# Optimization experiments

Measured on AMD Instinct MI355X. Metric: run time of the kernel, lower is better.

The kernel has to match this reference:

```python
import jax, jax.numpy as jnp
import numpy as np

HIDDEN = 1024
HEADS = 16
HEAD_DIM = HIDDEN // HEADS
ROPE_THETA = 10000.0
WINDOW = 128
NEG_INF = -1e9


def _rope_cos_sin(seq_len, head_dim, theta, dtype):
    # inv_freq: [dh/2]; emb = concat([freqs, freqs]) to match rotate-half convention
    inv_freq = 1.0 / (theta ** (jnp.arange(0, head_dim, 2, dtype=jnp.float32) / head_dim))
    pos = jnp.arange(seq_len, dtype=jnp.float32)
    freqs = jnp.einsum('s,d->sd', pos, inv_freq)          # [S, dh/2]
    emb = jnp.concatenate([freqs, freqs], axis=-1)        # [S, dh]
    return jnp.cos(emb).astype(dtype), jnp.sin(emb).astype(dtype)


def _apply_rope(x, cos, sin):
    # x: [B, S, H, dh]; cos/sin: [S, dh] broadcast over batch and heads
    x1, x2 = jnp.split(x, 2, axis=-1)
    half_rot = jnp.concatenate([-x2, x1], axis=-1)
    c = cos[None, :, None, :]
    s = sin[None, :, None, :]
    return x * c + half_rot * s


def setup_inputs() -> dict:
    key = jax.random.key(0)
    k1, k2, k3, k4, k5 = jax.random.split(key, 5)
    std = 0.02
    return {
        'hidden_states': jax.random.normal(k1, (2, 2048, HIDDEN), dtype=jnp.float32),
        'Wq': jax.random.normal(k2, (HIDDEN, HEADS, HEAD_DIM), dtype=jnp.float32) * std,
        'Wk': jax.random.normal(k3, (HIDDEN, HEADS, HEAD_DIM), dtype=jnp.float32) * std,
        'Wv': jax.random.normal(k4, (HIDDEN, HEADS, HEAD_DIM), dtype=jnp.float32) * std,
        'Wo': jax.random.normal(k5, (HEADS, HEAD_DIM, HIDDEN), dtype=jnp.float32) * std,
    }


def reference(hidden_states, Wq, Wk, Wv, Wo):
    B, S, D = hidden_states.shape
    x4 = hidden_states.reshape(B, S, HEADS, HEAD_DIM)
    cos, sin = _rope_cos_sin(S, HEAD_DIM, ROPE_THETA, hidden_states.dtype)
    # RoPE applied to raw hidden states (pre-projection), per original module
    q_in = _apply_rope(x4, cos, sin).reshape(B, S, D)
    k_in = q_in  # query and key get identical RoPE of the same tensor
    v_in = hidden_states

    q = jnp.einsum('bsd,dhk->bshk', q_in, Wq)  # [B,S,H,dh]
    k = jnp.einsum('bsd,dhk->bshk', k_in, Wk)
    v = jnp.einsum('bsd,dhk->bshk', v_in, Wv)

    scale = 1.0 / jnp.sqrt(jnp.asarray(HEAD_DIM, dtype=q.dtype))
    scores = jnp.einsum('bqhd,bkhd->bhqk', q, k) * scale  # [B,H,S,S]

    # sliding-window mask: |i - j| < WINDOW
    pos = jnp.arange(S)
    win = jnp.abs(pos[:, None] - pos[None, :]) < WINDOW   # [S,S] bool
    scores = jnp.where(win[None, None, :, :], scores, NEG_INF)

    probs = jax.nn.softmax(scores, axis=-1)
    out = jnp.einsum('bhqk,bkhd->bqhd', probs, v)          # [B,S,H,dh]
    return jnp.einsum('bqhd,hdo->bqo', out, Wo)            # [B,S,D]
```

## Files before the change

kernel.cpp:

```cpp
#include <hip/hip_runtime.h>
#include <hip/hip_bf16.h>
#include <cstdint>
#include <cmath>

typedef __bf16 bf16_t;
typedef __bf16 bf16x8 __attribute__((ext_vector_type(8)));
typedef __bf16 bf16x4 __attribute__((ext_vector_type(4)));
typedef float  f32x4  __attribute__((ext_vector_type(4)));

#define MFMA16(a, b, c) __builtin_amdgcn_mfma_f32_16x16x32_bf16(a, b, c, 0, 0, 0)

constexpr int   SS    = 2048;
constexpr int   DD    = 1024;
constexpr int   HH    = 16;
constexpr float SCALE = 0.125f;
constexpr float L2E   = 1.44269504088896f;

__device__ __forceinline__ bool detect_fp32(const uint16_t* w) {
    uint16_t v = w[threadIdx.x & 63];
    int e = (v >> 7) & 0xFF;
    unsigned long long m = __ballot(e >= 0x80);
    return __popcll(m) >= 4;
}

__device__ __forceinline__ float ldin(const void* p, size_t i, bool f32) {
    return f32 ? ((const float*)p)[i] : (float)((const bf16_t*)p)[i];
}

__device__ __forceinline__ void gload_lds16(const bf16_t* g, bf16_t* l) {
    __builtin_amdgcn_global_load_lds(
        (const __attribute__((address_space(1))) void*)(g),
        (__attribute__((address_space(3))) void*)(l), 16, 0, 0);
}

__global__ __launch_bounds__(256) void prep_kernel(
    const void* __restrict__ hidden, const void* __restrict__ Wq,
    const void* __restrict__ Wk, const void* __restrict__ Wv,
    const void* __restrict__ Wo,
    bf16_t* __restrict__ roped, bf16_t* __restrict__ hiddenb,
    bf16_t* __restrict__ WqT, bf16_t* __restrict__ WkT,
    bf16_t* __restrict__ WvT, bf16_t* __restrict__ WoT) {
    const bool f32 = detect_fp32((const uint16_t*)Wq);
    __shared__ bf16_t tile[32][33];
    if (blockIdx.x < 1024) {
        int gid = blockIdx.x * 256 + threadIdx.x;
        int ic = (gid & 3) * 8;
        int h  = (gid >> 2) & 15;
        int s  = (gid >> 6) & 2047;
        int b  = gid >> 17;
        size_t base = ((size_t)(b * SS + s)) * DD + h * 64 + ic;
        float x[8], y[8];
        if (f32) {
            const float* hp = (const float*)hidden;
            f32x4 x0 = *(const f32x4*)(hp + base);
            f32x4 x1 = *(const f32x4*)(hp + base + 4);
            f32x4 y0 = *(const f32x4*)(hp + base + 32);
            f32x4 y1 = *(const f32x4*)(hp + base + 36);
#pragma unroll
            for (int j = 0; j < 4; ++j) {
                x[j] = x0[j]; x[4 + j] = x1[j];
                y[j] = y0[j]; y[4 + j] = y1[j];
            }
        } else {
            const bf16_t* hp = (const bf16_t*)hidden;
            bf16x8 xv = *(const bf16x8*)(hp + base);
            bf16x8 yv = *(const bf16x8*)(hp + base + 32);
#pragma unroll
            for (int j = 0; j < 8; ++j) { x[j] = (float)xv[j]; y[j] = (float)yv[j]; }
        }
        bf16x8 ro, rh;
#pragma unroll
        for (int j = 0; j < 8; ++j) {
            int i = ic + j;
            float invf = exp2f(-(float)i * (13.287712379549449f / 32.0f));
            float sn, cs;
            __sincosf((float)s * invf, &sn, &cs);
            ro[j]  = (bf16_t)(x[j] * cs - y[j] * sn);
            rh[j]  = (bf16_t)(y[j] * cs + x[j] * sn);
        }
        *(bf16x8*)(roped + base)      = ro;
        *(bf16x8*)(roped + base + 32) = rh;
        if (f32) {
            bf16x8 hb0, hb1;
#pragma unroll
            for (int j = 0; j < 8; ++j) { hb0[j] = (bf16_t)x[j]; hb1[j] = (bf16_t)y[j]; }
            *(bf16x8*)(hiddenb + base)      = hb0;
            *(bf16x8*)(hiddenb + base + 32) = hb1;
        }
    } else {
        int w = blockIdx.x - 1024;
        int z = w >> 10;
        int yy = (w >> 5) & 31, xx = w & 31;
        const void* src = (z == 0) ? Wq : (z == 1) ? Wk : (z == 2) ? Wv : Wo;
        bf16_t*     dst = (z == 0) ? WqT : (z == 1) ? WkT : (z == 2) ? WvT : WoT;
        int tx = threadIdx.x & 31, ty = threadIdx.x >> 5;
        int x0 = xx * 32, y0 = yy * 32;
#pragma unroll
        for (int j = 0; j < 4; ++j)
            tile[ty + j * 8][tx] =
                (bf16_t)ldin(src, (size_t)(y0 + ty + j * 8) * DD + x0 + tx, f32);
        __syncthreads();
#pragma unroll
        for (int j = 0; j < 4; ++j)
            dst[(size_t)(x0 + ty + j * 8) * DD + y0 + tx] = tile[tx][ty + j * 8];
    }
}

__device__ __forceinline__ void stage_a128(const bf16_t* A, int m0, int k0,
                                           bf16_t* As, int tid) {
#pragma unroll
    for (int i = 0; i < 4; ++i) {
        int c = tid + i * 256;
        int r = c >> 3, g = (c & 7) ^ (r & 7);
        gload_lds16(A + (size_t)(m0 + r) * DD + k0 + g * 8, As + c * 8);
    }
}
__device__ __forceinline__ void stage_b64(const bf16_t* Bt, int n0, int k0,
                                          bf16_t* Bs, int tid) {
#pragma unroll
    for (int i = 0; i < 2; ++i) {
        int c = tid + i * 256;
        int r = c >> 3, g = (c & 7) ^ (r & 7);
        gload_lds16(Bt + (size_t)(n0 + r) * DD + k0 + g * 8, Bs + c * 8);
    }
}

__global__ __launch_bounds__(256, 4) void gemm_qkv_fused(
    const bf16_t* __restrict__ roped, const void* __restrict__ hidden_raw,
    const bf16_t* __restrict__ hiddenb, const uint16_t* __restrict__ wdet,
    const bf16_t* __restrict__ WqT, const bf16_t* __restrict__ WkT,
    const bf16_t* __restrict__ WvT,
    bf16_t* __restrict__ Qo, bf16_t* __restrict__ Ko, bf16_t* __restrict__ Vt) {
    __shared__ __align__(16) bf16_t As[128 * 64];
    __shared__ __align__(16) bf16_t B1[64 * 64];
    __shared__ __align__(16) bf16_t B2[64 * 64];
    const int tid = threadIdx.x, lane = tid & 63, quad = lane >> 4, l16 = lane & 15;
    const int wave = tid >> 6, wm = (wave >> 1) * 64, wn = (wave & 1) * 32;
    const int sw = l16 & 7;

    const int lin = blockIdx.x;
    const int z   = lin & 1;
    const int p   = lin >> 1;
    const int xcd = p & 7, rem = p >> 3;
    const int mb  = (xcd >> 1) * 8 + (rem >> 3);
    const int nb  = (xcd & 1) * 8 + (rem & 7);
    const int m0  = mb * 128, n0 = nb * 64;

    f32x4 acc1[4][2], acc2[4][2];
#pragma unroll
    for (int i = 0; i < 4; ++i)
#pragma unroll
        for (int j = 0; j < 2; ++j) { acc1[i][j] = (f32x4)0.0f; acc2[i][j] = (f32x4)0.0f; }

    if (z == 0) {
        for (int k0 = 0; k0 < DD; k0 += 64) {
            stage_a128(roped, m0, k0, As, tid);
            stage_b64(WqT, n0, k0, B1, tid);
            stage_b64(WkT, n0, k0, B2, tid);
            __syncthreads();
#pragma unroll
            for (int half = 0; half < 2; ++half) {
                const int h4 = half * 4;
                bf16x8 af[4], b1f[2], b2f[2];
#pragma unroll
                for (int t = 0; t < 4; ++t)
                    af[t] = *(const bf16x8*)(As + (wm + t * 16 + l16) * 64 + ((h4 + quad) ^ sw) * 8);
#pragma unroll
                for (int t = 0; t < 2; ++t) {
                    b1f[t] = *(const bf16x8*)(B1 + (wn + t * 16 + l16) * 64 + ((h4 + quad) ^ sw) * 8);
                    b2f[t] = *(const bf16x8*)(B2 + (wn + t * 16 + l16) * 64 + ((h4 + quad) ^ sw) * 8);
                }
#pragma unroll
                for (int i = 0; i < 4; ++i)
#pragma unroll
                    for (int j = 0; j < 2; ++j) {
                        acc1[i][j] = MFMA16(af[i], b1f[j], acc1[i][j]);
                        acc2[i][j] = MFMA16(af[i], b2f[j], acc2[i][j]);
                    }
            }
            __syncthreads();
        }
#pragma unroll
        for (int i = 0; i < 4; ++i) {
            int mbase = m0 + wm + i * 16 + quad * 4;
            int b = mbase >> 11, sl = mbase & 2047;
#pragma unroll
            for (int j = 0; j < 2; ++j) {
                int d = wn + j * 16 + l16;
                size_t base = (((size_t)b * HH + nb) * SS + sl) * 64 + d;
#pragma unroll
                for (int r = 0; r < 4; ++r) {
                    Qo[base + 64 * r] = (bf16_t)acc1[i][j][r];
                    Ko[base + 64 * r] = (bf16_t)acc2[i][j][r];
                }
            }
        }
    } else {
        const bool f32 = detect_fp32(wdet);
        const bf16_t* A = f32 ? hiddenb : (const bf16_t*)hidden_raw;
        for (int k0 = 0; k0 < DD; k0 += 64) {
            stage_a128(A, m0, k0, As, tid);
            stage_b64(WvT, n0, k0, B1, tid);
            __syncthreads();
#pragma unroll
            for (int half = 0; half < 2; ++half) {
                const int h4 = half * 4;
                bf16x8 af[4], b1f[2];
#pragma unroll
                for (int t = 0; t < 4; ++t)
                    af[t] = *(const bf16x8*)(As + (wm + t * 16 + l16) * 64 + ((h4 + quad) ^ sw) * 8);
#pragma unroll
                for (int t = 0; t < 2; ++t)
                    b1f[t] = *(const bf16x8*)(B1 + (wn + t * 16 + l16) * 64 + ((h4 + quad) ^ sw) * 8);
#pragma unroll
                for (int i = 0; i < 4; ++i)
#pragma unroll
                    for (int j = 0; j < 2; ++j)
                        acc1[i][j] = MFMA16(af[i], b1f[j], acc1[i][j]);
            }
            __syncthreads();
        }
#pragma unroll
        for (int i = 0; i < 4; ++i) {
            int mbase = m0 + wm + i * 16 + quad * 4;
            int b = mbase >> 11, sl = mbase & 2047;
#pragma unroll
            for (int j = 0; j < 2; ++j) {
                int d = wn + j * 16 + l16;
                bf16x4 v;
                v[0] = (bf16_t)acc1[i][j][0]; v[1] = (bf16_t)acc1[i][j][1];
                v[2] = (bf16_t)acc1[i][j][2]; v[3] = (bf16_t)acc1[i][j][3];
                *(bf16x4*)(Vt + (((size_t)b * HH + nb) * 64 + d) * SS + sl) = v;
            }
        }
    }
}

__global__ __launch_bounds__(256) void attn_kernel(
    const bf16_t* __restrict__ Q, const bf16_t* __restrict__ Kk,
    const bf16_t* __restrict__ Vt, bf16_t* __restrict__ attn) {
    __shared__ __align__(16) bf16_t Ks[2][32 * 64];
    __shared__ __align__(16) bf16_t Vs[2][64 * 32];
    __shared__ __align__(16) bf16_t Pl[4][16 * 40];
    const int tid = threadIdx.x, wave = tid >> 6, lane = tid & 63;
    const int quad = lane >> 4, l16 = lane & 15;
    const int sw7 = l16 & 7, sw3 = l16 & 3;

    int lin = (blockIdx.x >> 3) + 128 * (blockIdx.x & 7);
    const int qb0 = (lin & 31) * 64;
    const int h   = (lin >> 5) & 15;
    const int b   = lin >> 9;
    const int qw  = qb0 + wave * 16;

    const size_t bh = (size_t)b * HH + h;
    const bf16_t* Qp = Q  + bh * SS * 64;
    const bf16_t* Kp = Kk + bh * SS * 64;
    const bf16_t* Vp = Vt + bh * 64 * SS;
    bf16_t* P = &Pl[wave][0];

    bf16x8 q0 = *(const bf16x8*)(Qp + (size_t)(qw + l16) * 64 + quad * 8);
    bf16x8 q1 = *(const bf16x8*)(Qp + (size_t)(qw + l16) * 64 + 32 + quad * 8);

    f32x4 Oacc[4];
#pragma unroll
    for (int t = 0; t < 4; ++t) Oacc[t] = (f32x4)0.0f;
    float lsum[4] = {0.f, 0.f, 0.f, 0.f};

    int lo = qb0 - 127; if (lo < 0) lo = 0; lo &= ~31;
    int hi = qb0 + 63 + 127; if (hi > SS - 1) hi = SS - 1;

    const int krow = tid >> 3, kcol = ((tid & 7) ^ (krow & 7)) * 8;
    const int vrow = tid >> 2, vcol = ((tid & 3) ^ (vrow & 3)) * 8;

    int parity = 0;
    for (int kt = lo; kt <= hi; kt += 32, parity ^= 1) {
        gload_lds16(Kp + (size_t)(kt + krow) * 64 + kcol, &Ks[parity][0] + tid * 8);
        gload_lds16(Vp + (size_t)vrow * SS + kt + vcol, &Vs[parity][0] + tid * 8);
        __syncthreads();

        const bf16_t* Kl = &Ks[parity][0];
        const bf16_t* Vl = &Vs[parity][0];
        bf16x8 k00 = *(const bf16x8*)(Kl + l16 * 64 + (quad ^ sw7) * 8);
        bf16x8 k01 = *(const bf16x8*)(Kl + l16 * 64 + ((quad + 4) ^ sw7) * 8);
        bf16x8 k10 = *(const bf16x8*)(Kl + (16 + l16) * 64 + (quad ^ sw7) * 8);
        bf16x8 k11 = *(const bf16x8*)(Kl + (16 + l16) * 64 + ((quad + 4) ^ sw7) * 8);
        bf16x8 vf[4];
#pragma unroll
        for (int t = 0; t < 4; ++t)
            vf[t] = *(const bf16x8*)(Vl + (t * 16 + l16) * 32 + (quad ^ sw3) * 8);

        f32x4 s0 = MFMA16(q0, k00, (f32x4)0.0f);  s0 = MFMA16(q1, k01, s0);
        f32x4 s1 = MFMA16(q0, k10, (f32x4)0.0f);  s1 = MFMA16(q1, k11, s1);

        const int kr0 = kt + l16, kr1 = kt + 16 + l16;
#pragma unroll
        for (int r = 0; r < 4; ++r) {
            int qa = qw + quad * 4 + r;
            int d0 = qa - kr0; if (d0 < 0) d0 = -d0;
            int d1 = qa - kr1; if (d1 < 0) d1 = -d1;
            float p0 = (d0 < 128) ? exp2f(s0[r] * (SCALE * L2E)) : 0.0f;
            float p1 = (d1 < 128) ? exp2f(s1[r] * (SCALE * L2E)) : 0.0f;
            lsum[r] += p0 + p1;
            P[(quad * 4 + r) * 40 + l16]      = (bf16_t)p0;
            P[(quad * 4 + r) * 40 + 16 + l16] = (bf16_t)p1;
        }
        __asm__ volatile("s_waitcnt lgkmcnt(0)" ::: "memory");
        bf16x8 pf = *(const bf16x8*)(P + l16 * 40 + quad * 8);
#pragma unroll
        for (int t = 0; t < 4; ++t)
            Oacc[t] = MFMA16(pf, vf[t], Oacc[t]);
    }

#pragma unroll
    for (int r = 0; r < 4; ++r) {
        float l = lsum[r];
        l += __shfl_xor(l, 1, 64);
        l += __shfl_xor(l, 2, 64);
        l += __shfl_xor(l, 4, 64);
        l += __shfl_xor(l, 8, 64);
        float inv = 1.0f / l;
        int sa = qw + quad * 4 + r;
        size_t base = (((size_t)b * SS + sa) * HH + h) * 64 + l16;
        attn[base]      = (bf16_t)(Oacc[0][r] * inv);
        attn[base + 16] = (bf16_t)(Oacc[1][r] * inv);
        attn[base + 32] = (bf16_t)(Oacc[2][r] * inv);
        attn[base + 48] = (bf16_t)(Oacc[3][r] * inv);
    }
}

__global__ __launch_bounds__(256, 4) void gemm_out_kernel(
    const bf16_t* __restrict__ A, const bf16_t* __restrict__ WoT,
    const uint16_t* __restrict__ wdet, void* __restrict__ out) {
    __shared__ __align__(16) bf16_t As[128 * 64];
    __shared__ __align__(16) bf16_t B1[64 * 64];
    const int tid = threadIdx.x, lane = tid & 63, quad = lane >> 4, l16 = lane & 15;
    const int wave = tid >> 6, wm = (wave >> 1) * 64, wn = (wave & 1) * 32;
    const int sw = l16 & 7;

    const int lin = blockIdx.x;
    const int xcd = lin & 7, s = lin >> 3;
    const int mb = (xcd >> 1) * 8 + (s >> 3);
    const int nb = (xcd & 1) * 8 + (s & 7);
    const int m0 = mb * 128, n0 = nb * 64;

    f32x4 acc[4][2];
#pragma unroll
    for (int i = 0; i < 4; ++i)
#pragma unroll
        for (int j = 0; j < 2; ++j) acc[i][j] = (f32x4)0.0f;

    for (int k0 = 0; k0 < DD; k0 += 64) {
        stage_a128(A, m0, k0, As, tid);
        stage_b64(WoT, n0, k0, B1, tid);
        __syncthreads();
#pragma unroll
        for (int half = 0; half < 2; ++half) {
            const int h4 = half * 4;
            bf16x8 af[4], b1f[2];
#pragma unroll
            for (int t = 0; t < 4; ++t)
                af[t] = *(const bf16x8*)(As + (wm + t * 16 + l16) * 64 + ((h4 + quad) ^ sw) * 8);
#pragma unroll
            for (int t = 0; t < 2; ++t)
                b1f[t] = *(const bf16x8*)(B1 + (wn + t * 16 + l16) * 64 + ((h4 + quad) ^ sw) * 8);
#pragma unroll
            for (int i = 0; i < 4; ++i)
#pragma unroll
                for (int j = 0; j < 2; ++j)
                    acc[i][j] = MFMA16(af[i], b1f[j], acc[i][j]);
        }
        __syncthreads();
    }

    const bool f32 = detect_fp32(wdet);
#pragma unroll
    for (int i = 0; i < 4; ++i) {
        int mbase = m0 + wm + i * 16 + quad * 4;
#pragma unroll
        for (int j = 0; j < 2; ++j) {
            int n = n0 + wn + j * 16 + l16;
#pragma unroll
            for (int r = 0; r < 4; ++r) {
                size_t idx = (size_t)(mbase + r) * DD + n;
                if (f32) ((float*)out)[idx] = acc[i][j][r];
                else     ((bf16_t*)out)[idx] = (bf16_t)acc[i][j][r];
            }
        }
    }
}

extern "C" void kernel_launch(void* const* d_in, const int* in_sizes, int n_in,
                              void* d_out, int out_size, void* d_ws, size_t ws_size,
                              hipStream_t stream) {
    const void* hidden = d_in[0];
    const void* Wq = d_in[1];
    const void* Wk = d_in[2];
    const void* Wv = d_in[3];
    const void* Wo = d_in[4];
    const uint16_t* wdet = (const uint16_t*)d_in[1];
    char* ws = (char*)d_ws;

    bf16_t* roped   = (bf16_t*)(ws);
    bf16_t* hiddenb = (bf16_t*)(ws + ( 8u << 20));
    bf16_t* WqT     = (bf16_t*)(ws + (16u << 20));
    bf16_t* WkT     = (bf16_t*)(ws + (18u << 20));
    bf16_t* WvT     = (bf16_t*)(ws + (20u << 20));
    bf16_t* WoT     = (bf16_t*)(ws + (22u << 20));
    bf16_t* Qb      = (bf16_t*)(ws + (24u << 20));
    bf16_t* Kb      = (bf16_t*)(ws + (32u << 20));
    bf16_t* Vt      = (bf16_t*)(ws + (40u << 20));
    bf16_t* attn    = roped;

    hipLaunchKernelGGL(prep_kernel, dim3(5120), dim3(256), 0, stream,
                       hidden, Wq, Wk, Wv, Wo, roped, hiddenb,
                       WqT, WkT, WvT, WoT);
    hipLaunchKernelGGL(gemm_qkv_fused, dim3(1024), dim3(256), 0, stream,
                       roped, hidden, hiddenb, wdet, WqT, WkT, WvT, Qb, Kb, Vt);
    hipLaunchKernelGGL(attn_kernel, dim3(1024), dim3(256), 0, stream,
                       Qb, Kb, Vt, attn);
    hipLaunchKernelGGL(gemm_out_kernel, dim3(512), dim3(256), 0, stream,
                       attn, WoT, wdet, d_out);
}
```

Before: 153.4 us.

## Retile QKV GEMM to uniform 128x128 tiles and add MFMA priority hints

The QKV projection kernel drops the mixed Q+K-fused and V blocks. Every block now computes a uniform 128x128 output tile for one of Q, K or V, over a 768-block grid, with each wave holding 4x4 accumulators. This balances the work per block and raises arithmetic intensity per LDS load, at the cost of more registers and a lower occupancy bound (3 blocks per CU instead of 4). The attention kernel also wraps its MFMA groups in s_setprio to favour the matrix-issuing waves.

Measured after the change: 157.8 us. 1.03x slower.

```diff
diff --git a/kernel.cpp b/kernel.cpp
--- a/kernel.cpp
+++ b/kernel.cpp
@@ -125,112 +125,92 @@
     }
 }
 
-__global__ __launch_bounds__(256, 4) void gemm_qkv_fused(
+__global__ __launch_bounds__(256, 3) void gemm_qkv(
     const bf16_t* __restrict__ roped, const void* __restrict__ hidden_raw,
     const bf16_t* __restrict__ hiddenb, const uint16_t* __restrict__ wdet,
     const bf16_t* __restrict__ WqT, const bf16_t* __restrict__ WkT,
     const bf16_t* __restrict__ WvT,
     bf16_t* __restrict__ Qo, bf16_t* __restrict__ Ko, bf16_t* __restrict__ Vt) {
     __shared__ __align__(16) bf16_t As[128 * 64];
-    __shared__ __align__(16) bf16_t B1[64 * 64];
-    __shared__ __align__(16) bf16_t B2[64 * 64];
+    __shared__ __align__(16) bf16_t Bs[128 * 64];
     const int tid = threadIdx.x, lane = tid & 63, quad = lane >> 4, l16 = lane & 15;
-    const int wave = tid >> 6, wm = (wave >> 1) * 64, wn = (wave & 1) * 32;
+    const int wave = tid >> 6, wm = (wave >> 1) * 64, wn = (wave & 1) * 64;
     const int sw = l16 & 7;
 
     const int lin = blockIdx.x;
-    const int z   = lin & 1;
-    const int p   = lin >> 1;
-    const int xcd = p & 7, rem = p >> 3;
-    const int mb  = (xcd >> 1) * 8 + (rem >> 3);
-    const int nb  = (xcd & 1) * 8 + (rem & 7);
-    const int m0  = mb * 128, n0 = nb * 64;
-
-    f32x4 acc1[4][2], acc2[4][2];
+    const int xcd = lin & 7;
+    const int t8  = lin >> 3;
+    const int z   = t8 >> 5;
+    const int mb  = t8 & 31;
+    const int m0  = mb * 128, n0 = xcd * 128;
+
+    const bf16_t* A;
+    const bf16_t* B;
+    if (z == 0)      { A = roped; B = WqT; }
+    else if (z == 1) { A = roped; B = WkT; }
+    else {
+        const bool f32 = detect_fp32(wdet);
+        A = f32 ? hiddenb : (const bf16_t*)hidden_raw;
+        B = WvT;
+    }
+
+    f32x4 acc[4][4];
 #pragma unroll
     for (int i = 0; i < 4; ++i)
 #pragma unroll
-        for (int j = 0; j < 2; ++j) { acc1[i][j] = (f32x4)0.0f; acc2[i][j] = (f32x4)0.0f; }
-
-    if (z == 0) {
-        for (int k0 = 0; k0 < DD; k0 += 64) {
-            stage_a128(roped, m0, k0, As, tid);
-            stage_b64(WqT, n0, k0, B1, tid);
-            stage_b64(WkT, n0, k0, B2, tid);
-            __syncthreads();
-#pragma unroll
-            for (int half = 0; half < 2; ++half) {
-                const int h4 = half * 4;
-                bf16x8 af[4], b1f[2], b2f[2];
-#pragma unroll
-                for (int t = 0; t < 4; ++t)
-                    af[t] = *(const bf16x8*)(As + (wm + t * 16 + l16) * 64 + ((h4 + quad) ^ sw) * 8);
-#pragma unroll
-                for (int t = 0; t < 2; ++t) {
-                    b1f[t] = *(const bf16x8*)(B1 + (wn + t * 16 + l16) * 64 + ((h4 + quad) ^ sw) * 8);
-                    b2f[t] = *(const bf16x8*)(B2 + (wn + t * 16 + l16) * 64 + ((h4 + quad) ^ sw) * 8);
-                }
-#pragma unroll
-                for (int i = 0; i < 4; ++i)
-#pragma unroll
-                    for (int j = 0; j < 2; ++j) {
-                        acc1[i][j] = MFMA16(af[i], b1f[j], acc1[i][j]);
-                        acc2[i][j] = MFMA16(af[i], b2f[j], acc2[i][j]);
-                    }
+        for (int j = 0; j < 4; ++j) acc[i][j] = (f32x4)0.0f;
+
+    for (int k0 = 0; k0 < DD; k0 += 64) {
+        stage_a128(A, m0, k0, As, tid);
+        stage_a128(B, n0, k0, Bs, tid);
+        __syncthreads();
+#pragma unroll
+        for (int half = 0; half < 2; ++half) {
+            const int h4 = half * 4;
+            bf16x8 af[4], bf[4];
+#pragma unroll
+            for (int t = 0; t < 4; ++t) {
+                af[t] = *(const bf16x8*)(As + (wm + t * 16 + l16) * 64 + ((h4 + quad) ^ sw) * 8);
+                bf[t] = *(const bf16x8*)(Bs + (wn + t * 16 + l16) * 64 + ((h4 + quad) ^ sw) * 8);
             }
-            __syncthreads();
-        }
+#pragma unroll
+            for (int i = 0; i < 4; ++i)
+#pragma unroll
+                for (int j = 0; j < 4; ++j)
+                    acc[i][j] = MFMA16(af[i], bf[j], acc[i][j]);
+        }
+        __syncthreads();
+    }
+
+    if (z < 2) {
+        bf16_t* O = (z == 0) ? Qo : Ko;
 #pragma unroll
         for (int i = 0; i < 4; ++i) {
             int mbase = m0 + wm + i * 16 + quad * 4;
             int b = mbase >> 11, sl = mbase & 2047;
 #pragma unroll
-            for (int j = 0; j < 2; ++j) {
-                int d = wn + j * 16 + l16;
-                size_t base = (((size_t)b * HH + nb) * SS + sl) * 64 + d;
-#pragma unroll
-                for (int r = 0; r < 4; ++r) {
-                    Qo[base + 64 * r] = (bf16_t)acc1[i][j][r];
-                    Ko[base + 64 * r] = (bf16_t)acc2[i][j][r];
-                }
+            for (int j = 0; j < 4; ++j) {
+                int n = n0 + wn + j * 16 + l16;
+                int h = n >> 6, d = n & 63;
+                size_t base = (((size_t)b * HH + h) * SS + sl) * 64 + d;
+#pragma unroll
+                for (int r = 0; r < 4; ++r)
+                    O[base + 64 * r] = (bf16_t)acc[i][j][r];
             }
         }
     } else {
-        const bool f32 = detect_fp32(wdet);
-        const bf16_t* A = f32 ? hiddenb : (const bf16_t*)hidden_raw;
-        for (int k0 = 0; k0 < DD; k0 += 64) {
-            stage_a128(A, m0, k0, As, tid);
-            stage_b64(WvT, n0, k0, B1, tid);
-            __syncthreads();
-#pragma unroll
-            for (int half = 0; half < 2; ++half) {
-                const int h4 = half * 4;
-                bf16x8 af[4], b1f[2];
-#pragma unroll
-                for (int t = 0; t < 4; ++t)
-                    af[t] = *(const bf16x8*)(As + (wm + t * 16 + l16) * 64 + ((h4 + quad) ^ sw) * 8);
-#pragma unroll
-                for (int t = 0; t < 2; ++t)
-                    b1f[t] = *(const bf16x8*)(B1 + (wn + t * 16 + l16) * 64 + ((h4 + quad) ^ sw) * 8);
-#pragma unroll
-                for (int i = 0; i < 4; ++i)
-#pragma unroll
-                    for (int j = 0; j < 2; ++j)
-                        acc1[i][j] = MFMA16(af[i], b1f[j], acc1[i][j]);
-            }
-            __syncthreads();
-        }
 #pragma unroll
         for (int i = 0; i < 4; ++i) {
             int mbase = m0 + wm + i * 16 + quad * 4;
             int b = mbase >> 11, sl = mbase & 2047;
 #pragma unroll
-            for (int j = 0; j < 2; ++j) {
-                int d = wn + j * 16 + l16;
+            for (int j = 0; j < 4; ++j) {
+                int n = n0 + wn + j * 16 + l16;
+                int h = n >> 6, d = n & 63;
                 bf16x4 v;
-                v[0] = (bf16_t)acc1[i][j][0]; v[1] = (bf16_t)acc1[i][j][1];
-                v[2] = (bf16_t)acc1[i][j][2]; v[3] = (bf16_t)acc1[i][j][3];
-                *(bf16x4*)(Vt + (((size_t)b * HH + nb) * 64 + d) * SS + sl) = v;
+                v[0] = (bf16_t)acc[i][j][0]; v[1] = (bf16_t)acc[i][j][1];
+                v[2] = (bf16_t)acc[i][j][2]; v[3] = (bf16_t)acc[i][j][3];
+                *(bf16x4*)(Vt + (((size_t)b * HH + h) * 64 + d) * SS + sl) = v;
             }
         }
     }
@@ -289,8 +269,10 @@
         for (int t = 0; t < 4; ++t)
             vf[t] = *(const bf16x8*)(Vl + (t * 16 + l16) * 32 + (quad ^ sw3) * 8);
 
+        __builtin_amdgcn_s_setprio(1);
         f32x4 s0 = MFMA16(q0, k00, (f32x4)0.0f);  s0 = MFMA16(q1, k01, s0);
         f32x4 s1 = MFMA16(q0, k10, (f32x4)0.0f);  s1 = MFMA16(q1, k11, s1);
+        __builtin_amdgcn_s_setprio(0);
 
         const int kr0 = kt + l16, kr1 = kt + 16 + l16;
 #pragma unroll
@@ -306,9 +288,11 @@
         }
         __asm__ volatile("s_waitcnt lgkmcnt(0)" ::: "memory");
         bf16x8 pf = *(const bf16x8*)(P + l16 * 40 + quad * 8);
+        __builtin_amdgcn_s_setprio(1);
 #pragma unroll
         for (int t = 0; t < 4; ++t)
             Oacc[t] = MFMA16(pf, vf[t], Oacc[t]);
+        __builtin_amdgcn_s_setprio(0);
     }
 
 #pragma unroll
@@ -414,7 +398,7 @@
     hipLaunchKernelGGL(prep_kernel, dim3(5120), dim3(256), 0, stream,
                        hidden, Wq, Wk, Wv, Wo, roped, hiddenb,
                        WqT, WkT, WvT, WoT);
-    hipLaunchKernelGGL(gemm_qkv_fused, dim3(1024), dim3(256), 0, stream,
+    hipLaunchKernelGGL(gemm_qkv, dim3(768), dim3(256), 0, stream,
                        roped, hidden, hiddenb, wdet, WqT, WkT, WvT, Qb, Kb, Vt);
     hipLaunchKernelGGL(attn_kernel, dim3(1024), dim3(256), 0, stream,
                        Qb, Kb, Vt, attn);
```
